# Performance work log

Hardware: AMD Instinct MI355X
Metric: run time of the kernel (lower is better)

Reference implementation:

```python
import jax, jax.numpy as jnp
import numpy as np

E, T, D, K = 8, 32768, 1024, 2  # experts, tokens, model dim, topk


def setup_inputs() -> dict:
    key = jax.random.key(0)
    k1, k2, k3, k4 = jax.random.split(key, 4)
    return {
        "tokens": jax.random.normal(k1, (T, D), jnp.float32),
        "router_w": jax.random.normal(k2, (E, D), jnp.float32) * 0.02,
        "w1": jax.random.normal(k3, (E, D, D), jnp.float32) * 0.02,
        "w2": jax.random.normal(k4, (E, D, D), jnp.float32) * 0.02,
    }


def reference(tokens, router_w, w1, w2):
    # Router: softmax over experts, then top-k (order of k irrelevant: combine is a sum)
    scores = jax.nn.softmax(tokens @ router_w.T, axis=-1)          # [T, E]
    topv, topi = jax.lax.top_k(scores, K)                          # [T, K]
    n_tok = tokens.shape[0]
    # Per-token gate weight for each expert (sum of topk weights where index==e).
    gate = jnp.zeros((n_tok, E), tokens.dtype).at[
        jnp.arange(n_tok)[:, None], topi
    ].add(topv)                                                    # [T, E]
    # Dense per-expert MLP, masked/weighted combine == sorted gather + scatter-sum
    out = jnp.zeros_like(tokens)
    for e in range(E):  # fixed small expert count; not a data-dim loop
        h = jax.nn.gelu(tokens @ w1[e], approximate=False)         # [T, D]
        out = out + gate[:, e:e + 1] * (h @ w2[e])                 # [T, D]
    return out
```

## Files before the change

### kernel.cpp

```cpp
#include <hip/hip_runtime.h>
#include <hip/hip_bf16.h>
#include <math.h>
#include <stdint.h>

#define TOK 32768
#define DIM 1024
#define NE 8
#define NSEG 16
#define BMCAP (2 * TOK + NSEG * 256)

#define C_CNT(s) ((s) * 16)
#define C_CUR(s) (256 + (s) * 16)
#define C_SEG(s) (512 + (s))

typedef __attribute__((ext_vector_type(8))) short bf16x8;
typedef __attribute__((ext_vector_type(4))) float f32x4;
typedef unsigned short ushort_t;

__device__ __forceinline__ unsigned short f2b(float x) {
  union { float f; unsigned u; } v; v.f = x;
  unsigned r = v.u + 0x7fffu + ((v.u >> 16) & 1u);
  return (unsigned short)(r >> 16);
}

__device__ __forceinline__ float b2f(unsigned short u) {
  union { unsigned u; float f; } v;
  v.u = ((unsigned)u) << 16;
  return v.f;
}

__device__ __forceinline__ float gelu_fast(float x) {
  const float y2 = -1.5957691216057308f * x * fmaf(0.044715f, x * x, 1.0f);
  return x * __builtin_amdgcn_rcpf(1.0f + __expf(y2));
}

__device__ __forceinline__ void async16(void* lds, const void* g) {
  auto* lp = (__attribute__((address_space(3))) uint32_t*)lds;
  auto* gp = (__attribute__((address_space(1))) uint32_t*)(const_cast<void*>(g));
  __builtin_amdgcn_global_load_lds(gp, lp, 16, 0, 0);
}

__global__ __launch_bounds__(256) void router_seq3(
    const float* __restrict__ tokens, const float* __restrict__ rw,
    int* __restrict__ topi, float* __restrict__ topv) {
  __shared__ float xs[2][32][132];
  __shared__ float wsh[2][8][132];
  __shared__ float sc[256];
  const int tid = threadIdx.x;
  const int e = tid & 7;
  const int tr = tid >> 3;
  const int t0 = blockIdx.x * 32;

  float4 lx0, lx1, lx2, lx3, lw;
  auto issue = [&](int c) {
    const int col = (tid & 31) * 4;
    lx0 = *(const float4*)&tokens[(size_t)(t0 + ((tid + 0) >> 5)) * DIM + c * 128 + col];
    lx1 = *(const float4*)&tokens[(size_t)(t0 + ((tid + 256) >> 5)) * DIM + c * 128 + col];
    lx2 = *(const float4*)&tokens[(size_t)(t0 + ((tid + 512) >> 5)) * DIM + c * 128 + col];
    lx3 = *(const float4*)&tokens[(size_t)(t0 + ((tid + 768) >> 5)) * DIM + c * 128 + col];
    lw  = *(const float4*)&rw[(size_t)(tid >> 5) * DIM + c * 128 + col];
  };
  auto commit = [&](int b) {
    const int col = (tid & 31) * 4;
    *(float4*)&xs[b][(tid + 0) >> 5][col] = lx0;
    *(float4*)&xs[b][(tid + 256) >> 5][col] = lx1;
    *(float4*)&xs[b][(tid + 512) >> 5][col] = lx2;
    *(float4*)&xs[b][(tid + 768) >> 5][col] = lx3;
    *(float4*)&wsh[b][tid >> 5][col] = lw;
  };

  issue(0);
  commit(0);
  __syncthreads();
  float s = 0.f;
  for (int c = 0; c < 8; c++) {
    const int b = c & 1;
    if (c + 1 < 8) issue(c + 1);
#pragma unroll
    for (int k4 = 0; k4 < 32; k4++) {
      const float4 xv = *(const float4*)&xs[b][tr][k4 * 4];
      const float4 wv = *(const float4*)&wsh[b][e][k4 * 4];
      s = fmaf(xv.x, wv.x, s);
      s = fmaf(xv.y, wv.y, s);
      s = fmaf(xv.z, wv.z, s);
      s = fmaf(xv.w, wv.w, s);
    }
    if (c + 1 < 8) commit(b ^ 1);
    __syncthreads();
  }
  sc[tid] = s;
  __syncthreads();
  if (e == 0) {
    float p[NE];
    float m = sc[tr * 8];
#pragma unroll
    for (int i = 1; i < NE; i++) m = fmaxf(m, sc[tr * 8 + i]);
    float sum = 0.f;
#pragma unroll
    for (int i = 0; i < NE; i++) {
      p[i] = expf(sc[tr * 8 + i] - m);
      sum += p[i];
    }
#pragma unroll
    for (int i = 0; i < NE; i++) p[i] = p[i] / sum;
    const int t = t0 + tr;
    int e0 = 0;
#pragma unroll
    for (int i = 1; i < NE; i++) if (p[i] > p[e0]) e0 = i;
    int e1 = (e0 == 0) ? 1 : 0;
#pragma unroll
    for (int i = 0; i < NE; i++) if (i != e0 && p[i] > p[e1]) e1 = i;
    topi[t * 2] = e0;     topv[t * 2] = p[e0];
    topi[t * 2 + 1] = e1; topv[t * 2 + 1] = p[e1];
  }
}

__global__ __launch_bounds__(256) void hist_kernel(const int* __restrict__ topi,
                                                   int* __restrict__ ctrl) {
  __shared__ int h[NSEG];
  const int tid = threadIdx.x;
  if (tid < NSEG) h[tid] = 0;
  __syncthreads();
  const int t = blockIdx.x * 256 + tid;
  atomicAdd(&h[topi[t * 2]], 1);
  atomicAdd(&h[8 + topi[t * 2 + 1]], 1);
  __syncthreads();
  if (tid < NSEG) atomicAdd(&ctrl[C_CNT(tid)], h[tid]);
}

__global__ void prefix_kernel(int* ctrl) {
  if (threadIdx.x == 0 && blockIdx.x == 0) {
    int s = 0;
    for (int g = 0; g < NSEG; g++) {
      ctrl[C_SEG(g)] = s;
      ctrl[C_CUR(g)] = s;
      s += (ctrl[C_CNT(g)] + 255) & ~255;
    }
    ctrl[C_SEG(NSEG)] = s;
  }
}

__global__ __launch_bounds__(256) void init_rows(int* __restrict__ row_token) {
  const int i = blockIdx.x * 256 + threadIdx.x;
  if (i < BMCAP) row_token[i] = TOK;
}

__global__ __launch_bounds__(256) void assign2(
    const int* __restrict__ topi, int* __restrict__ ctrl,
    int* __restrict__ row_token, int* __restrict__ inv) {
  __shared__ int h[NSEG];
  __shared__ int base[NSEG];
  const int tid = threadIdx.x;
  const int t = blockIdx.x * 256 + tid;
  if (tid < NSEG) h[tid] = 0;
  __syncthreads();
  const int s0 = topi[t * 2], s1 = 8 + topi[t * 2 + 1];
  const int o0 = atomicAdd(&h[s0], 1);
  const int o1 = atomicAdd(&h[s1], 1);
  __syncthreads();
  if (tid < NSEG) base[tid] = atomicAdd(&ctrl[C_CUR(tid)], h[tid]);
  __syncthreads();
  const int p0 = base[s0] + o0, p1 = base[s1] + o1;
  row_token[p0] = t; inv[t * 2] = p0;
  row_token[p1] = t; inv[t * 2 + 1] = p1;
}

__global__ __launch_bounds__(256) void cast_tokens(
    const float* __restrict__ t, ushort_t* __restrict__ x16) {
  const size_t i = ((size_t)blockIdx.x * 256 + threadIdx.x) * 8;
  const float4 a = *(const float4*)(t + i);
  const float4 b = *(const float4*)(t + i + 4);
  bf16x8 h;
  h[0] = (short)f2b(a.x); h[1] = (short)f2b(a.y);
  h[2] = (short)f2b(a.z); h[3] = (short)f2b(a.w);
  h[4] = (short)f2b(b.x); h[5] = (short)f2b(b.y);
  h[6] = (short)f2b(b.z); h[7] = (short)f2b(b.w);
  *(bf16x8*)(x16 + i) = h;
}

__global__ __launch_bounds__(256) void transpose_cast(
    const float* __restrict__ w, ushort_t* __restrict__ wT) {
  __shared__ float tile[64][65];
  const int e = blockIdx.z;
  const int n0 = blockIdx.x * 64, k0 = blockIdx.y * 64;
  const int tx = threadIdx.x & 63, ty = threadIdx.x >> 6;
  const float* src = w + ((size_t)e << 20);
  ushort_t* dst = wT + ((size_t)e << 20);
#pragma unroll
  for (int r = ty; r < 64; r += 4)
    tile[r][tx] = src[(size_t)(k0 + r) * DIM + n0 + tx];
  __syncthreads();
#pragma unroll
  for (int r = ty; r < 64; r += 4)
    dst[(size_t)(n0 + r) * DIM + k0 + tx] = f2b(tile[tx][r]);
}

__global__ __launch_bounds__(256) void combine(
    const ushort_t* __restrict__ gY, const int* __restrict__ inv,
    const float* __restrict__ topv, float* __restrict__ out) {
  const size_t i = (size_t)blockIdx.x * 256 + threadIdx.x;
  const int t = (int)(i >> 7);
  const int c = (int)(i & 127) << 3;
  const int s0 = inv[t * 2], s1 = inv[t * 2 + 1];
  const float g0 = topv[t * 2], g1 = topv[t * 2 + 1];
  const bf16x8 y0 = *(const bf16x8*)&gY[(size_t)s0 * DIM + c];
  const bf16x8 y1 = *(const bf16x8*)&gY[(size_t)s1 * DIM + c];
  f32x4 o0, o1;
#pragma unroll
  for (int j = 0; j < 4; j++)
    o0[j] = g0 * b2f((unsigned short)y0[j]) + g1 * b2f((unsigned short)y1[j]);
#pragma unroll
  for (int j = 0; j < 4; j++)
    o1[j] = g0 * b2f((unsigned short)y0[4 + j]) +
            g1 * b2f((unsigned short)y1[4 + j]);
  float* op = out + (size_t)t * DIM + c;
  *(f32x4*)op = o0;
  *(f32x4*)(op + 4) = o1;
}

template <int PASS>
__global__ __launch_bounds__(512, 4) void dgemm(
    const ushort_t* __restrict__ Asrc, const ushort_t* __restrict__ Wt,
    const int* __restrict__ row_token, const int* __restrict__ ctrl, int s_lo,
    int s_hi, int chunk, ushort_t* __restrict__ Hout) {
  const int l = (blockIdx.x & 7) * chunk + (blockIdx.x >> 3);
  const int mt = l >> 3, nt = l & 7;
  const int rbase0 = ctrl[C_SEG(s_lo)];
  const int rend = ctrl[C_SEG(s_hi)];
  const int m0 = rbase0 + mt * 256;
  if (m0 >= rend) return;
  const int n0 = nt * 128;
  int sg = s_lo;
  for (int i = s_lo + 1; i < s_hi; i++)
    if (m0 >= ctrl[C_SEG(i)]) sg = i;
  const int e = sg & 7;
  const ushort_t* B = Wt + ((size_t)e << 20);

  __shared__ __align__(16) char smem[49152];
  ushort_t (*As)[8192] = (ushort_t(*)[8192])smem;
  ushort_t (*Bs)[4096] = (ushort_t(*)[4096])(smem + 32768);
  float* scratch = (float*)smem;

  const int tid = threadIdx.x;
  const int lane = tid & 63;
  const int wave = tid >> 6;
  const int wm = wave >> 1, wn = wave & 1;
  const int lr = lane & 15;
  const int kx = (((lane >> 4) ^ (lr & 3) ^ ((lr >> 2) & 3)) << 3);

  const int ko = (((lane & 3) ^ ((lane >> 2) & 3) ^ ((lane >> 4) & 3)) << 3);
  const int ar0 = wave * 32 + (lane >> 2);
  const int brr = wave * 16 + (lane >> 2);
  const ushort_t *asrc0, *asrc1, *bsrc;
  if (PASS == 0) {
    int tk0 = row_token[m0 + ar0];
    int tk1 = row_token[m0 + ar0 + 16];
    if (tk0 >= TOK) tk0 = 0;
    if (tk1 >= TOK) tk1 = 0;
    asrc0 = Asrc + (size_t)tk0 * DIM + ko;
    asrc1 = Asrc + (size_t)tk1 * DIM + ko;
  } else {
    asrc0 = Asrc + (size_t)(m0 + ar0) * DIM + ko;
    asrc1 = Asrc + (size_t)(m0 + ar0 + 16) * DIM + ko;
  }
  bsrc = B + (size_t)(n0 + brr) * DIM + ko;

  f32x4 acc[4][4] = {};

  auto stage = [&](int b, int k0) {
    async16(&As[b][wave * 1024], asrc0 + k0);
    async16(&As[b][wave * 1024 + 512], asrc1 + k0);
    async16(&Bs[b][wave * 512], bsrc + k0);
  };
  auto compute = [&](int b) {
    bf16x8 a[4], bb[4];
#pragma unroll
    for (int mi = 0; mi < 4; mi++)
      a[mi] = *(const bf16x8*)&As[b][(wm * 64 + mi * 16 + lr) * 32 + kx];
#pragma unroll
    for (int ni = 0; ni < 4; ni++)
      bb[ni] = *(const bf16x8*)&Bs[b][(wn * 64 + ni * 16 + lr) * 32 + kx];
#pragma unroll
    for (int mi = 0; mi < 4; mi++)
#pragma unroll
      for (int ni = 0; ni < 4; ni++)
        acc[mi][ni] = __builtin_amdgcn_mfma_f32_16x16x32_bf16(
            a[mi], bb[ni], acc[mi][ni], 0, 0, 0);
  };

  stage(0, 0);
  __syncthreads();
  int cur = 0;
#pragma unroll 1
  for (int t = 0; t < 31; t++) {
    stage(cur ^ 1, (t + 1) * 32);
    compute(cur);
    __syncthreads();
    cur ^= 1;
  }
  compute(cur);
  __syncthreads();

  const int grow = (lane >> 4) << 2;
  const int erow = tid >> 3;
  const int ec0 = (tid & 7) * 16;
#pragma unroll 1
  for (int rnd = 0; rnd < 4; rnd++) {
    if (wm == rnd) {
#pragma unroll
      for (int mi = 0; mi < 4; mi++) {
#pragma unroll
        for (int ni = 0; ni < 4; ni++) {
#pragma unroll
          for (int r = 0; r < 4; r++) {
            const int lrow = mi * 16 + grow + r;
            const int lcol = (wn * 64 + ni * 16 + lr) ^ ((lrow & 3) << 2);
            scratch[lrow * 128 + lcol] = acc[mi][ni][r];
          }
        }
      }
    }
    __syncthreads();
    {
      const int q = (erow & 3) << 2;
      f32x4 v[4];
#pragma unroll
      for (int k = 0; k < 4; k++)
        v[k] = *(const f32x4*)&scratch[erow * 128 + ((ec0 + 4 * k) ^ q)];
      const int rr = m0 + rnd * 64 + erow;
      bf16x8 h0, h1;
      if (PASS == 0) {
#pragma unroll
        for (int k = 0; k < 2; k++)
#pragma unroll
          for (int j = 0; j < 4; j++)
            h0[k * 4 + j] = (short)f2b(gelu_fast(v[k][j]));
#pragma unroll
        for (int k = 0; k < 2; k++)
#pragma unroll
          for (int j = 0; j < 4; j++)
            h1[k * 4 + j] = (short)f2b(gelu_fast(v[2 + k][j]));
      } else {
#pragma unroll
        for (int k = 0; k < 2; k++)
#pragma unroll
          for (int j = 0; j < 4; j++) h0[k * 4 + j] = (short)f2b(v[k][j]);
#pragma unroll
        for (int k = 0; k < 2; k++)
#pragma unroll
          for (int j = 0; j < 4; j++) h1[k * 4 + j] = (short)f2b(v[2 + k][j]);
      }
      *(bf16x8*)&Hout[(size_t)rr * DIM + n0 + ec0] = h0;
      *(bf16x8*)&Hout[(size_t)rr * DIM + n0 + ec0 + 8] = h1;
    }
    __syncthreads();
  }
}

extern "C" void kernel_launch(void* const* d_in, const int* in_sizes, int n_in,
                              void* d_out, int out_size, void* d_ws,
                              size_t ws_size, hipStream_t stream) {
  (void)in_sizes; (void)n_in; (void)ws_size; (void)out_size;
  const float* tokens = (const float*)d_in[0];
  const float* rw = (const float*)d_in[1];
  const float* w1 = (const float*)d_in[2];
  const float* w2 = (const float*)d_in[3];
  float* out = (float*)d_out;

  char* ws = (char*)d_ws;
  size_t off = 0;
  auto alloc = [&](size_t b) {
    size_t o = off;
    off += (b + 255) & ~(size_t)255;
    return o;
  };
  int* ctrl = (int*)(ws + alloc(4096));
  int* topi = (int*)(ws + alloc((size_t)TOK * 2 * 4));
  float* topv = (float*)(ws + alloc((size_t)TOK * 2 * 4));
  int* inv = (int*)(ws + alloc((size_t)TOK * 2 * 4));
  int* row_token = (int*)(ws + alloc((size_t)BMCAP * 4));
  ushort_t* w2T = (ushort_t*)(ws + alloc((size_t)NE * DIM * DIM * 2));
  ushort_t* H = (ushort_t*)(ws + alloc((size_t)BMCAP * DIM * 2));
  const size_t region = alloc((size_t)BMCAP * DIM * 2);
  ushort_t* X16 = (ushort_t*)(ws + region);
  ushort_t* w1T = (ushort_t*)(ws + region + (size_t)TOK * DIM * 2);
  ushort_t* gY = (ushort_t*)(ws + region);

  hipMemsetAsync(ctrl, 0, 4096, stream);
  router_seq3<<<TOK / 32, 256, 0, stream>>>(tokens, rw, topi, topv);
  hist_kernel<<<TOK / 256, 256, 0, stream>>>(topi, ctrl);
  prefix_kernel<<<1, 64, 0, stream>>>(ctrl);
  init_rows<<<BMCAP / 256, 256, 0, stream>>>(row_token);
  assign2<<<TOK / 256, 256, 0, stream>>>(topi, ctrl, row_token, inv);
  cast_tokens<<<TOK * DIM / 8 / 256, 256, 0, stream>>>(tokens, X16);
  dim3 tg(16, 16, 8);
  transpose_cast<<<tg, 256, 0, stream>>>(w1, w1T);
  transpose_cast<<<tg, 256, 0, stream>>>(w2, w2T);
  dgemm<0><<<2176, 512, 0, stream>>>(X16, w1T, row_token, ctrl, 0, NSEG, 272,
                                     H);
  dgemm<1><<<2176, 512, 0, stream>>>(H, w2T, row_token, ctrl, 0, NSEG, 272,
                                     gY);
  combine<<<TOK * (DIM / 8) / 256, 256, 0, stream>>>(gY, inv, topv, out);
}
```

Measured before the change: 539.4 us.

## Fuse token bf16 cast into router and use 4-wave dgemm with 64x128 warp tiles

The router kernel now writes the bf16 copy of the tokens while it already has them in registers, so the separate cast_tokens launch and its extra full read of the fp32 tokens are gone. The grouped GEMM drops from 8 waves to 4 waves per 256x128 block. Each wave now computes a 64x128 tile with 32 accumulators, which cuts LDS B-fragment reads per MFMA and raises register reuse. The cost is higher register pressure, fewer waves to hide latency (launch bounds 256,2), and more load instructions per wave.

```diff
diff --git a/kernel.cpp b/kernel.cpp
--- a/kernel.cpp
+++ b/kernel.cpp
@@ -15,6 +15,7 @@
 
 typedef __attribute__((ext_vector_type(8))) short bf16x8;
 typedef __attribute__((ext_vector_type(4))) float f32x4;
+typedef __attribute__((ext_vector_type(4))) unsigned short u16x4;
 typedef unsigned short ushort_t;
 
 __device__ __forceinline__ unsigned short f2b(float x) {
@@ -42,7 +43,8 @@
 
 __global__ __launch_bounds__(256) void router_seq3(
     const float* __restrict__ tokens, const float* __restrict__ rw,
-    int* __restrict__ topi, float* __restrict__ topv) {
+    int* __restrict__ topi, float* __restrict__ topv,
+    ushort_t* __restrict__ x16) {
   __shared__ float xs[2][32][132];
   __shared__ float wsh[2][8][132];
   __shared__ float sc[256];
@@ -68,9 +70,22 @@
     *(float4*)&xs[b][(tid + 768) >> 5][col] = lx3;
     *(float4*)&wsh[b][tid >> 5][col] = lw;
   };
+  auto commitX = [&](int c) {
+    const int col = c * 128 + (tid & 31) * 4;
+    u16x4 u;
+    u[0] = f2b(lx0.x); u[1] = f2b(lx0.y); u[2] = f2b(lx0.z); u[3] = f2b(lx0.w);
+    *(u16x4*)&x16[(size_t)(t0 + ((tid + 0) >> 5)) * DIM + col] = u;
+    u[0] = f2b(lx1.x); u[1] = f2b(lx1.y); u[2] = f2b(lx1.z); u[3] = f2b(lx1.w);
+    *(u16x4*)&x16[(size_t)(t0 + ((tid + 256) >> 5)) * DIM + col] = u;
+    u[0] = f2b(lx2.x); u[1] = f2b(lx2.y); u[2] = f2b(lx2.z); u[3] = f2b(lx2.w);
+    *(u16x4*)&x16[(size_t)(t0 + ((tid + 512) >> 5)) * DIM + col] = u;
+    u[0] = f2b(lx3.x); u[1] = f2b(lx3.y); u[2] = f2b(lx3.z); u[3] = f2b(lx3.w);
+    *(u16x4*)&x16[(size_t)(t0 + ((tid + 768) >> 5)) * DIM + col] = u;
+  };
 
   issue(0);
   commit(0);
+  commitX(0);
   __syncthreads();
   float s = 0.f;
   for (int c = 0; c < 8; c++) {
@@ -85,7 +100,10 @@
       s = fmaf(xv.z, wv.z, s);
       s = fmaf(xv.w, wv.w, s);
     }
-    if (c + 1 < 8) commit(b ^ 1);
+    if (c + 1 < 8) {
+      commit(b ^ 1);
+      commitX(c + 1);
+    }
     __syncthreads();
   }
   sc[tid] = s;
@@ -163,19 +181,6 @@
   const int p0 = base[s0] + o0, p1 = base[s1] + o1;
   row_token[p0] = t; inv[t * 2] = p0;
   row_token[p1] = t; inv[t * 2 + 1] = p1;
-}
-
-__global__ __launch_bounds__(256) void cast_tokens(
-    const float* __restrict__ t, ushort_t* __restrict__ x16) {
-  const size_t i = ((size_t)blockIdx.x * 256 + threadIdx.x) * 8;
-  const float4 a = *(const float4*)(t + i);
-  const float4 b = *(const float4*)(t + i + 4);
-  bf16x8 h;
-  h[0] = (short)f2b(a.x); h[1] = (short)f2b(a.y);
-  h[2] = (short)f2b(a.z); h[3] = (short)f2b(a.w);
-  h[4] = (short)f2b(b.x); h[5] = (short)f2b(b.y);
-  h[6] = (short)f2b(b.z); h[7] = (short)f2b(b.w);
-  *(bf16x8*)(x16 + i) = h;
 }
 
 __global__ __launch_bounds__(256) void transpose_cast(
@@ -219,7 +224,7 @@
 }
 
 template <int PASS>
-__global__ __launch_bounds__(512, 4) void dgemm(
+__global__ __launch_bounds__(256, 2) void dgemm(
     const ushort_t* __restrict__ Asrc, const ushort_t* __restrict__ Wt,
     const int* __restrict__ row_token, const int* __restrict__ ctrl, int s_lo,
     int s_hi, int chunk, ushort_t* __restrict__ Hout) {
@@ -244,46 +249,51 @@
   const int tid = threadIdx.x;
   const int lane = tid & 63;
   const int wave = tid >> 6;
-  const int wm = wave >> 1, wn = wave & 1;
   const int lr = lane & 15;
   const int kx = (((lane >> 4) ^ (lr & 3) ^ ((lr >> 2) & 3)) << 3);
-
   const int ko = (((lane & 3) ^ ((lane >> 2) & 3) ^ ((lane >> 4) & 3)) << 3);
-  const int ar0 = wave * 32 + (lane >> 2);
-  const int brr = wave * 16 + (lane >> 2);
-  const ushort_t *asrc0, *asrc1, *bsrc;
-  if (PASS == 0) {
-    int tk0 = row_token[m0 + ar0];
-    int tk1 = row_token[m0 + ar0 + 16];
-    if (tk0 >= TOK) tk0 = 0;
-    if (tk1 >= TOK) tk1 = 0;
-    asrc0 = Asrc + (size_t)tk0 * DIM + ko;
-    asrc1 = Asrc + (size_t)tk1 * DIM + ko;
-  } else {
-    asrc0 = Asrc + (size_t)(m0 + ar0) * DIM + ko;
-    asrc1 = Asrc + (size_t)(m0 + ar0 + 16) * DIM + ko;
-  }
-  bsrc = B + (size_t)(n0 + brr) * DIM + ko;
-
-  f32x4 acc[4][4] = {};
+
+  const ushort_t* asrc[4];
+  const ushort_t* bsrc[2];
+#pragma unroll
+  for (int j = 0; j < 4; j++) {
+    const int rA = wave * 64 + j * 16 + (lane >> 2);
+    if (PASS == 0) {
+      int tk = row_token[m0 + rA];
+      if (tk >= TOK) tk = 0;
+      asrc[j] = Asrc + (size_t)tk * DIM + ko;
+    } else {
+      asrc[j] = Asrc + (size_t)(m0 + rA) * DIM + ko;
+    }
+  }
+#pragma unroll
+  for (int j = 0; j < 2; j++) {
+    const int rB = wave * 32 + j * 16 + (lane >> 2);
+    bsrc[j] = B + (size_t)(n0 + rB) * DIM + ko;
+  }
+
+  f32x4 acc[4][8] = {};
 
   auto stage = [&](int b, int k0) {
-    async16(&As[b][wave * 1024], asrc0 + k0);
-    async16(&As[b][wave * 1024 + 512], asrc1 + k0);
-    async16(&Bs[b][wave * 512], bsrc + k0);
+#pragma unroll
+    for (int j = 0; j < 4; j++)
+      async16(&As[b][wave * 2048 + j * 512], asrc[j] + k0);
+#pragma unroll
+    for (int j = 0; j < 2; j++)
+      async16(&Bs[b][wave * 1024 + j * 512], bsrc[j] + k0);
   };
   auto compute = [&](int b) {
-    bf16x8 a[4], bb[4];
+    bf16x8 a[4], bb[8];
 #pragma unroll
     for (int mi = 0; mi < 4; mi++)
-      a[mi] = *(const bf16x8*)&As[b][(wm * 64 + mi * 16 + lr) * 32 + kx];
-#pragma unroll
-    for (int ni = 0; ni < 4; ni++)
-      bb[ni] = *(const bf16x8*)&Bs[b][(wn * 64 + ni * 16 + lr) * 32 + kx];
+      a[mi] = *(const bf16x8*)&As[b][(wave * 64 + mi * 16 + lr) * 32 + kx];
+#pragma unroll
+    for (int ni = 0; ni < 8; ni++)
+      bb[ni] = *(const bf16x8*)&Bs[b][(ni * 16 + lr) * 32 + kx];
 #pragma unroll
     for (int mi = 0; mi < 4; mi++)
 #pragma unroll
-      for (int ni = 0; ni < 4; ni++)
+      for (int ni = 0; ni < 8; ni++)
         acc[mi][ni] = __builtin_amdgcn_mfma_f32_16x16x32_bf16(
             a[mi], bb[ni], acc[mi][ni], 0, 0, 0);
   };
@@ -302,19 +312,19 @@
   __syncthreads();
 
   const int grow = (lane >> 4) << 2;
-  const int erow = tid >> 3;
-  const int ec0 = (tid & 7) * 16;
+  const int erow = tid >> 2;
+  const int ec0 = (tid & 3) * 32;
 #pragma unroll 1
   for (int rnd = 0; rnd < 4; rnd++) {
-    if (wm == rnd) {
+    if (wave == rnd) {
 #pragma unroll
       for (int mi = 0; mi < 4; mi++) {
 #pragma unroll
-        for (int ni = 0; ni < 4; ni++) {
+        for (int ni = 0; ni < 8; ni++) {
 #pragma unroll
           for (int r = 0; r < 4; r++) {
             const int lrow = mi * 16 + grow + r;
-            const int lcol = (wn * 64 + ni * 16 + lr) ^ ((lrow & 3) << 2);
+            const int lcol = (ni * 16 + lr) ^ ((lrow & 3) << 2);
             scratch[lrow * 128 + lcol] = acc[mi][ni][r];
           }
         }
@@ -323,35 +333,30 @@
     __syncthreads();
     {
       const int q = (erow & 3) << 2;
-      f32x4 v[4];
-#pragma unroll
-      for (int k = 0; k < 4; k++)
+      f32x4 v[8];
+#pragma unroll
+      for (int k = 0; k < 8; k++)
         v[k] = *(const f32x4*)&scratch[erow * 128 + ((ec0 + 4 * k) ^ q)];
       const int rr = m0 + rnd * 64 + erow;
-      bf16x8 h0, h1;
-      if (PASS == 0) {
-#pragma unroll
-        for (int k = 0; k < 2; k++)
+      ushort_t* dst = &Hout[(size_t)rr * DIM + n0 + ec0];
+#pragma unroll
+      for (int half = 0; half < 4; half++) {
+        bf16x8 h;
+        if (PASS == 0) {
 #pragma unroll
           for (int j = 0; j < 4; j++)
-            h0[k * 4 + j] = (short)f2b(gelu_fast(v[k][j]));
-#pragma unroll
-        for (int k = 0; k < 2; k++)
+            h[j] = (short)f2b(gelu_fast(v[half * 2][j]));
 #pragma unroll
           for (int j = 0; j < 4; j++)
-            h1[k * 4 + j] = (short)f2b(gelu_fast(v[2 + k][j]));
-      } else {
-#pragma unroll
-        for (int k = 0; k < 2; k++)
-#pragma unroll
-          for (int j = 0; j < 4; j++) h0[k * 4 + j] = (short)f2b(v[k][j]);
-#pragma unroll
-        for (int k = 0; k < 2; k++)
-#pragma unroll
-          for (int j = 0; j < 4; j++) h1[k * 4 + j] = (short)f2b(v[2 + k][j]);
+            h[4 + j] = (short)f2b(gelu_fast(v[half * 2 + 1][j]));
+        } else {
+#pragma unroll
+          for (int j = 0; j < 4; j++) h[j] = (short)f2b(v[half * 2][j]);
+#pragma unroll
+          for (int j = 0; j < 4; j++) h[4 + j] = (short)f2b(v[half * 2 + 1][j]);
+        }
+        *(bf16x8*)(dst + half * 8) = h;
       }
-      *(bf16x8*)&Hout[(size_t)rr * DIM + n0 + ec0] = h0;
-      *(bf16x8*)&Hout[(size_t)rr * DIM + n0 + ec0 + 8] = h1;
     }
     __syncthreads();
   }
@@ -387,18 +392,17 @@
   ushort_t* gY = (ushort_t*)(ws + region);
 
   hipMemsetAsync(ctrl, 0, 4096, stream);
-  router_seq3<<<TOK / 32, 256, 0, stream>>>(tokens, rw, topi, topv);
+  router_seq3<<<TOK / 32, 256, 0, stream>>>(tokens, rw, topi, topv, X16);
   hist_kernel<<<TOK / 256, 256, 0, stream>>>(topi, ctrl);
   prefix_kernel<<<1, 64, 0, stream>>>(ctrl);
   init_rows<<<BMCAP / 256, 256, 0, stream>>>(row_token);
   assign2<<<TOK / 256, 256, 0, stream>>>(topi, ctrl, row_token, inv);
-  cast_tokens<<<TOK * DIM / 8 / 256, 256, 0, stream>>>(tokens, X16);
   dim3 tg(16, 16, 8);
   transpose_cast<<<tg, 256, 0, stream>>>(w1, w1T);
   transpose_cast<<<tg, 256, 0, stream>>>(w2, w2T);
-  dgemm<0><<<2176, 512, 0, stream>>>(X16, w1T, row_token, ctrl, 0, NSEG, 272,
+  dgemm<0><<<2176, 256, 0, stream>>>(X16, w1T, row_token, ctrl, 0, NSEG, 272,
                                      H);
-  dgemm<1><<<2176, 512, 0, stream>>>(H, w2T, row_token, ctrl, 0, NSEG, 272,
+  dgemm<1><<<2176, 256, 0, stream>>>(H, w2T, row_token, ctrl, 0, NSEG, 272,
                                      gY);
   combine<<<TOK * (DIM / 8) / 256, 256, 0, stream>>>(gY, inv, topv, out);
 }
```

Result: faster. 522.4 us (-3.1%).
